# Performance work log

Measured on AMD Instinct MI355X. Metric: run time of the kernel, lower is better.

Reference implementation:

```python
import jax, jax.numpy as jnp
import numpy as np
import itertools

LUT_DIM = 33  # 33x33x33 color LUT, as in Generator3DLUT_zero(dim=33)


def setup_inputs() -> dict:
    key = jax.random.key(0)
    k1, k2 = jax.random.split(key)
    # RGB image batch in [0,1]: [B, 3, H, W]
    x = jax.random.uniform(k1, (4, 3, 1080, 1920), dtype=jnp.float32)
    # Learned LUT parameter: [3, dim, dim, dim] (channels, b-axis, g-axis, r-axis)
    LUT = jax.random.normal(k2, (3, LUT_DIM, LUT_DIM, LUT_DIM), dtype=jnp.float32)
    return {"x": x, "LUT": LUT}


def _trilinear_lut(x, LUT, dim):
    # x: [B,3,H,W] in [0,1]; LUT: [3,dim,dim,dim] indexed [channel, b, g, r]
    # (r varies fastest, matching the original CUDA trilinear_forward kernel
    #  where flat index = r + g*dim + b*dim*dim).
    scaled = jnp.clip(x, 0.0, 1.0) * (dim - 1)          # [B,3,H,W]
    idx = jnp.clip(jnp.floor(scaled).astype(jnp.int32), 0, dim - 2)
    frac = scaled - idx.astype(scaled.dtype)            # in [0,1]
    r_id, g_id, b_id = idx[:, 0], idx[:, 1], idx[:, 2]   # each [B,H,W]
    fr, fg, fb = frac[:, 0], frac[:, 1], frac[:, 2]      # each [B,H,W]

    out = jnp.zeros_like(x)  # [B,3,H,W]
    for dr, dg, db in itertools.product((0, 1), repeat=3):  # 8 corners
        w = (jnp.where(dr, fr, 1.0 - fr)
             * jnp.where(dg, fg, 1.0 - fg)
             * jnp.where(db, fb, 1.0 - fb))               # [B,H,W]
        corner = LUT[:, b_id + db, g_id + dg, r_id + dr]  # [3,B,H,W] gather
        out = out + w[:, None] * jnp.transpose(corner, (1, 0, 2, 3))
    return out


def reference(x, LUT):
    return _trilinear_lut(x, LUT, LUT_DIM)
```

## Files before the change

kernel.cpp:

```cpp
#include <hip/hip_runtime.h>

#define DIM  33
#define DIM2 1089
#define DIM3 35937
#define HW   2073600
#define HW4  518400
#define NPIX 8294400
#define GROUPS (NPIX / 4)
#define CHUNK  4096
#define NCHUNK ((GROUPS + CHUNK - 1) / CHUNK)
#define LDS_BYTES (DIM3 * 4)
#define MAIN_BLOCKS  256
#define MAIN_THREADS 1024

typedef float vf4 __attribute__((ext_vector_type(4)));

#define TBL_OFF 64

__device__ __forceinline__ float ub(unsigned v, int b) {
    return (float)((v >> (8 * b)) & 0xffu);
}

__global__ __launch_bounds__(256) void lut_maxabs_kernel(
        const float* __restrict__ lut, unsigned* __restrict__ maxbits) {
    int i = blockIdx.x * 256 + threadIdx.x;
    float m = 0.0f;
    if (i < 3 * DIM3) m = fabsf(lut[i]);
#pragma unroll
    for (int off = 32; off > 0; off >>= 1)
        m = fmaxf(m, __shfl_down(m, off, 64));
    if ((threadIdx.x & 63) == 0)
        atomicMax(maxbits, __float_as_uint(m));
}

__global__ __launch_bounds__(256) void pack_lut_u8_kernel(
        const float* __restrict__ lut, const unsigned* __restrict__ maxbits,
        unsigned* __restrict__ tbl) {
    int i = blockIdx.x * 256 + threadIdx.x;
    if (i >= DIM3) return;
    float mx  = fmaxf(__uint_as_float(*maxbits), 1e-20f);
    float inv = 127.0f / mx;
    int q0 = min(max(__float2int_rn(lut[i]            * inv) + 128, 0), 255);
    int q1 = min(max(__float2int_rn(lut[i + DIM3]     * inv) + 128, 0), 255);
    int q2 = min(max(__float2int_rn(lut[i + 2 * DIM3] * inv) + 128, 0), 255);
    tbl[i] = (unsigned)q0 | ((unsigned)q1 << 8) | ((unsigned)q2 << 16);
}

extern __shared__ unsigned s_tbl[];

__global__ __launch_bounds__(MAIN_THREADS, 1) void lut_apply_lds(
        const float* __restrict__ x, const unsigned* __restrict__ tbl,
        unsigned* __restrict__ ctr, const unsigned* __restrict__ maxbits,
        float* __restrict__ out) {
    __shared__ unsigned chunk_s;
    for (int i = threadIdx.x; i < DIM3; i += MAIN_THREADS)
        s_tbl[i] = tbl[i];
    __syncthreads();

    const float mx   = fmaxf(__uint_as_float(*maxbits), 1e-20f);
    const float s_   = mx * (1.0f / 127.0f);
    const float bias = -128.0f * s_;

    for (;;) {
        if (threadIdx.x == 0) chunk_s = atomicAdd(ctr, 1u);
        __syncthreads();
        unsigned c = chunk_s;
        __syncthreads();
        if (c >= NCHUNK) return;

        int gend = min((int)((c + 1) * CHUNK), GROUPS);
        for (int g = (int)(c * CHUNK) + threadIdx.x; g < gend; g += MAIN_THREADS) {
            int n   = g / HW4;
            int rem = g - n * HW4;
            size_t base = (size_t)n * (size_t)(3 * HW) + (size_t)rem * 4;

            const vf4 rv = __builtin_nontemporal_load((const vf4*)(x + base));
            const vf4 gv = __builtin_nontemporal_load((const vf4*)(x + base + HW));
            const vf4 bv = __builtin_nontemporal_load((const vf4*)(x + base + 2 * (size_t)HW));

            float oa[4], ob[4], oc[4];
#pragma unroll
            for (int k = 0; k < 4; ++k) {
                float rs = fminf(fmaxf(rv[k], 0.0f), 1.0f) * 32.0f;
                float gs = fminf(fmaxf(gv[k], 0.0f), 1.0f) * 32.0f;
                float bs = fminf(fmaxf(bv[k], 0.0f), 1.0f) * 32.0f;
                int ri = min((int)rs, 31);
                int gi = min((int)gs, 31);
                int bi = min((int)bs, 31);
                float fr = rs - (float)ri;
                float fg = gs - (float)gi;
                float fb = bs - (float)bi;

                int i00 = bi * DIM2 + gi * DIM + ri;
                unsigned c000 = s_tbl[i00];
                unsigned c001 = s_tbl[i00 + 1];
                unsigned c010 = s_tbl[i00 + DIM];
                unsigned c011 = s_tbl[i00 + DIM + 1];
                unsigned c100 = s_tbl[i00 + DIM2];
                unsigned c101 = s_tbl[i00 + DIM2 + 1];
                unsigned c110 = s_tbl[i00 + DIM2 + DIM];
                unsigned c111 = s_tbl[i00 + DIM2 + DIM + 1];

                float wr1 = fr, wr0 = 1.0f - fr;
                float wg1 = fg, wg0 = 1.0f - fg;
                float wb1 = fb, wb0 = 1.0f - fb;
                float wb0g0 = wb0 * wg0, wb0g1 = wb0 * wg1;
                float wb1g0 = wb1 * wg0, wb1g1 = wb1 * wg1;
                float w000 = wb0g0 * wr0, w001 = wb0g0 * wr1;
                float w010 = wb0g1 * wr0, w011 = wb0g1 * wr1;
                float w100 = wb1g0 * wr0, w101 = wb1g0 * wr1;
                float w110 = wb1g1 * wr0, w111 = wb1g1 * wr1;

                float a0, a1, a2;
                a0 =      w000 * ub(c000, 0);
                a1 =      w000 * ub(c000, 1);
                a2 =      w000 * ub(c000, 2);
                a0 = fmaf(w001,  ub(c001, 0), a0);
                a1 = fmaf(w001,  ub(c001, 1), a1);
                a2 = fmaf(w001,  ub(c001, 2), a2);
                a0 = fmaf(w010,  ub(c010, 0), a0);
                a1 = fmaf(w010,  ub(c010, 1), a1);
                a2 = fmaf(w010,  ub(c010, 2), a2);
                a0 = fmaf(w011,  ub(c011, 0), a0);
                a1 = fmaf(w011,  ub(c011, 1), a1);
                a2 = fmaf(w011,  ub(c011, 2), a2);
                a0 = fmaf(w100,  ub(c100, 0), a0);
                a1 = fmaf(w100,  ub(c100, 1), a1);
                a2 = fmaf(w100,  ub(c100, 2), a2);
                a0 = fmaf(w101,  ub(c101, 0), a0);
                a1 = fmaf(w101,  ub(c101, 1), a1);
                a2 = fmaf(w101,  ub(c101, 2), a2);
                a0 = fmaf(w110,  ub(c110, 0), a0);
                a1 = fmaf(w110,  ub(c110, 1), a1);
                a2 = fmaf(w110,  ub(c110, 2), a2);
                a0 = fmaf(w111,  ub(c111, 0), a0);
                a1 = fmaf(w111,  ub(c111, 1), a1);
                a2 = fmaf(w111,  ub(c111, 2), a2);

                oa[k] = fmaf(s_, a0, bias);
                ob[k] = fmaf(s_, a1, bias);
                oc[k] = fmaf(s_, a2, bias);
            }
            vf4 s0 = {oa[0], oa[1], oa[2], oa[3]};
            vf4 s1 = {ob[0], ob[1], ob[2], ob[3]};
            vf4 s2 = {oc[0], oc[1], oc[2], oc[3]};
            __builtin_nontemporal_store(s0, (vf4*)(out + base));
            __builtin_nontemporal_store(s1, (vf4*)(out + base + HW));
            __builtin_nontemporal_store(s2, (vf4*)(out + base + 2 * (size_t)HW));
        }
    }
}

union F4H { vf4 f4; _Float16 h[8]; };

__global__ __launch_bounds__(256) void pack_lut8_kernel(
        const float* __restrict__ lut, vf4* __restrict__ lut8) {
    int i = blockIdx.x * blockDim.x + threadIdx.x;
    if (i >= DIM3) return;
    int b   = i / DIM2;
    int rem = i - b * DIM2;
    int g   = rem / DIM;
    int r   = rem - g * DIM;
    int b1 = min(b + 1, DIM - 1);
    int g1 = min(g + 1, DIM - 1);
    int r1 = min(r + 1, DIM - 1);
    _Float16 h[32];
#pragma unroll
    for (int db = 0; db < 2; ++db)
#pragma unroll
        for (int dg = 0; dg < 2; ++dg)
#pragma unroll
            for (int dr = 0; dr < 2; ++dr) {
                int bb = db ? b1 : b;
                int gg = dg ? g1 : g;
                int rr = dr ? r1 : r;
                int base = bb * DIM2 + gg * DIM + rr;
                int ci = ((db * 2 + dg) * 2 + dr) * 3;
                h[ci + 0] = (_Float16)lut[base];
                h[ci + 1] = (_Float16)lut[base + DIM3];
                h[ci + 2] = (_Float16)lut[base + 2 * DIM3];
            }
#pragma unroll
    for (int k = 24; k < 32; ++k) h[k] = (_Float16)0.0f;
    const vf4* hv = (const vf4*)h;
    vf4* dst = lut8 + (size_t)i * 4;
    dst[0] = hv[0]; dst[1] = hv[1]; dst[2] = hv[2]; dst[3] = hv[3];
}

__global__ __launch_bounds__(256) void lut_apply_fp16x8(
        const float* __restrict__ x, const vf4* __restrict__ lut8,
        float* __restrict__ out) {
    int i4 = blockIdx.x * blockDim.x + threadIdx.x;
    if (i4 >= NPIX / 4) return;
    int n   = i4 / HW4;
    int rem = i4 - n * HW4;
    size_t base = (size_t)n * (size_t)(3 * HW) + (size_t)rem * 4;
    const vf4 rv = __builtin_nontemporal_load((const vf4*)(x + base));
    const vf4 gv = __builtin_nontemporal_load((const vf4*)(x + base + HW));
    const vf4 bv = __builtin_nontemporal_load((const vf4*)(x + base + 2 * (size_t)HW));
    float oa[4], ob[4], oc[4];
#pragma unroll
    for (int k = 0; k < 4; ++k) {
        float rs = fminf(fmaxf(rv[k], 0.0f), 1.0f) * 32.0f;
        float gs = fminf(fmaxf(gv[k], 0.0f), 1.0f) * 32.0f;
        float bs = fminf(fmaxf(bv[k], 0.0f), 1.0f) * 32.0f;
        int ri = min((int)rs, 31);
        int gi = min((int)gs, 31);
        int bi = min((int)bs, 31);
        float fr = rs - (float)ri;
        float fg = gs - (float)gi;
        float fb = bs - (float)bi;
        const vf4* e = lut8 + (size_t)(bi * DIM2 + gi * DIM + ri) * 4;
        F4H q0, q1, q2;
        q0.f4 = e[0]; q1.f4 = e[1]; q2.f4 = e[2];
        float c[24];
#pragma unroll
        for (int j = 0; j < 8; ++j) {
            c[j] = (float)q0.h[j]; c[8 + j] = (float)q1.h[j]; c[16 + j] = (float)q2.h[j];
        }
        float wr[2] = {1.0f - fr, fr};
        float wg[2] = {1.0f - fg, fg};
        float wb[2] = {1.0f - fb, fb};
        float a0 = 0.0f, a1 = 0.0f, a2 = 0.0f;
#pragma unroll
        for (int db = 0; db < 2; ++db)
#pragma unroll
            for (int dg = 0; dg < 2; ++dg) {
                float wbg = wb[db] * wg[dg];
#pragma unroll
                for (int dr = 0; dr < 2; ++dr) {
                    float w = wbg * wr[dr];
                    int ci = ((db * 2 + dg) * 2 + dr) * 3;
                    a0 = fmaf(w, c[ci + 0], a0);
                    a1 = fmaf(w, c[ci + 1], a1);
                    a2 = fmaf(w, c[ci + 2], a2);
                }
            }
        oa[k] = a0; ob[k] = a1; oc[k] = a2;
    }
    vf4 s0 = {oa[0], oa[1], oa[2], oa[3]};
    vf4 s1 = {ob[0], ob[1], ob[2], ob[3]};
    vf4 s2 = {oc[0], oc[1], oc[2], oc[3]};
    __builtin_nontemporal_store(s0, (vf4*)(out + base));
    __builtin_nontemporal_store(s1, (vf4*)(out + base + HW));
    __builtin_nontemporal_store(s2, (vf4*)(out + base + 2 * (size_t)HW));
}

extern "C" void kernel_launch(void* const* d_in, const int* in_sizes, int n_in,
                              void* d_out, int out_size, void* d_ws, size_t ws_size,
                              hipStream_t stream) {
    const float* x   = (const float*)d_in[0];
    const float* lut = (const float*)d_in[1];
    float* out = (float*)d_out;

    unsigned* ctr     = (unsigned*)d_ws;
    unsigned* maxbits = (unsigned*)d_ws + 1;
    unsigned* tbl     = (unsigned*)((char*)d_ws + TBL_OFF);

    static hipError_t attr_err = hipFuncSetAttribute(
        (const void*)lut_apply_lds,
        hipFuncAttributeMaxDynamicSharedMemorySize, LDS_BYTES);
    hipError_t err2 = hipFuncSetAttribute(
        (const void*)lut_apply_lds,
        hipFuncAttributeMaxDynamicSharedMemorySize, LDS_BYTES);

    if (attr_err == hipSuccess && err2 == hipSuccess) {
        hipMemsetAsync(d_ws, 0, 8, stream);
        lut_maxabs_kernel<<<(3 * DIM3 + 255) / 256, 256, 0, stream>>>(lut, maxbits);
        pack_lut_u8_kernel<<<(DIM3 + 255) / 256, 256, 0, stream>>>(lut, maxbits, tbl);
        lut_apply_lds<<<MAIN_BLOCKS, MAIN_THREADS, LDS_BYTES, stream>>>(
            x, tbl, ctr, maxbits, out);
    } else {
        vf4* lut8 = (vf4*)((char*)d_ws + TBL_OFF);
        pack_lut8_kernel<<<(DIM3 + 255) / 256, 256, 0, stream>>>(lut, lut8);
        lut_apply_fp16x8<<<(GROUPS + 255) / 256, 256, 0, stream>>>(x, lut8, out);
    }
}
```

Measured before the change: 202.6 us.

## Fold LUT quantization into main kernel and drop memset and dynamic chunk scheduler

Replaces the memset, the atomic max-abs kernel and the separate pack kernel with a per-block max kernel that writes partial maxima to slots. The main kernel now reduces those maxima itself and quantizes the LUT straight into LDS. The atomic chunk counter is also replaced by a static grid-stride loop. This removes two launches plus the per-chunk barriers and atomics. In exchange every block repeats the LUT quantization from global memory, and static scheduling can leave some blocks finishing later than others.

Measured after the change: 188.1 us. -7.2%, faster.

```diff
diff --git a/kernel.cpp b/kernel.cpp
--- a/kernel.cpp
+++ b/kernel.cpp
@@ -7,11 +7,10 @@
 #define HW4  518400
 #define NPIX 8294400
 #define GROUPS (NPIX / 4)
-#define CHUNK  4096
-#define NCHUNK ((GROUPS + CHUNK - 1) / CHUNK)
 #define LDS_BYTES (DIM3 * 4)
 #define MAIN_BLOCKS  256
 #define MAIN_THREADS 1024
+#define NB_MAX ((3 * DIM3 + 255) / 256)
 
 typedef float vf4 __attribute__((ext_vector_type(4)));
 
@@ -21,133 +20,131 @@
     return (float)((v >> (8 * b)) & 0xffu);
 }
 
-__global__ __launch_bounds__(256) void lut_maxabs_kernel(
-        const float* __restrict__ lut, unsigned* __restrict__ maxbits) {
+__global__ __launch_bounds__(256) void lut_maxabs_blocks(
+        const float* __restrict__ lut, float* __restrict__ slots) {
+    __shared__ float red[4];
     int i = blockIdx.x * 256 + threadIdx.x;
     float m = 0.0f;
     if (i < 3 * DIM3) m = fabsf(lut[i]);
 #pragma unroll
     for (int off = 32; off > 0; off >>= 1)
         m = fmaxf(m, __shfl_down(m, off, 64));
-    if ((threadIdx.x & 63) == 0)
-        atomicMax(maxbits, __float_as_uint(m));
-}
-
-__global__ __launch_bounds__(256) void pack_lut_u8_kernel(
-        const float* __restrict__ lut, const unsigned* __restrict__ maxbits,
-        unsigned* __restrict__ tbl) {
-    int i = blockIdx.x * 256 + threadIdx.x;
-    if (i >= DIM3) return;
-    float mx  = fmaxf(__uint_as_float(*maxbits), 1e-20f);
-    float inv = 127.0f / mx;
-    int q0 = min(max(__float2int_rn(lut[i]            * inv) + 128, 0), 255);
-    int q1 = min(max(__float2int_rn(lut[i + DIM3]     * inv) + 128, 0), 255);
-    int q2 = min(max(__float2int_rn(lut[i + 2 * DIM3] * inv) + 128, 0), 255);
-    tbl[i] = (unsigned)q0 | ((unsigned)q1 << 8) | ((unsigned)q2 << 16);
+    if ((threadIdx.x & 63) == 0) red[threadIdx.x >> 6] = m;
+    __syncthreads();
+    if (threadIdx.x == 0)
+        slots[blockIdx.x] = fmaxf(fmaxf(red[0], red[1]), fmaxf(red[2], red[3]));
 }
 
 extern __shared__ unsigned s_tbl[];
 
 __global__ __launch_bounds__(MAIN_THREADS, 1) void lut_apply_lds(
-        const float* __restrict__ x, const unsigned* __restrict__ tbl,
-        unsigned* __restrict__ ctr, const unsigned* __restrict__ maxbits,
-        float* __restrict__ out) {
-    __shared__ unsigned chunk_s;
-    for (int i = threadIdx.x; i < DIM3; i += MAIN_THREADS)
-        s_tbl[i] = tbl[i];
+        const float* __restrict__ x, const float* __restrict__ lut,
+        const float* __restrict__ slots, float* __restrict__ out) {
+    __shared__ float red[16];
+
+    float m = 0.0f;
+    if (threadIdx.x < NB_MAX) m = slots[threadIdx.x];
+#pragma unroll
+    for (int off = 32; off > 0; off >>= 1)
+        m = fmaxf(m, __shfl_down(m, off, 64));
+    if ((threadIdx.x & 63) == 0) red[threadIdx.x >> 6] = m;
     __syncthreads();
-
-    const float mx   = fmaxf(__uint_as_float(*maxbits), 1e-20f);
+    float mx = red[0];
+#pragma unroll
+    for (int j = 1; j < 16; ++j) mx = fmaxf(mx, red[j]);
+    mx = fmaxf(mx, 1e-20f);
+
+    const float inv = 127.0f / mx;
+    for (int i = threadIdx.x; i < DIM3; i += MAIN_THREADS) {
+        int q0 = min(max(__float2int_rn(lut[i]            * inv) + 128, 0), 255);
+        int q1 = min(max(__float2int_rn(lut[i + DIM3]     * inv) + 128, 0), 255);
+        int q2 = min(max(__float2int_rn(lut[i + 2 * DIM3] * inv) + 128, 0), 255);
+        s_tbl[i] = (unsigned)q0 | ((unsigned)q1 << 8) | ((unsigned)q2 << 16);
+    }
+    __syncthreads();
+
     const float s_   = mx * (1.0f / 127.0f);
     const float bias = -128.0f * s_;
 
-    for (;;) {
-        if (threadIdx.x == 0) chunk_s = atomicAdd(ctr, 1u);
-        __syncthreads();
-        unsigned c = chunk_s;
-        __syncthreads();
-        if (c >= NCHUNK) return;
-
-        int gend = min((int)((c + 1) * CHUNK), GROUPS);
-        for (int g = (int)(c * CHUNK) + threadIdx.x; g < gend; g += MAIN_THREADS) {
-            int n   = g / HW4;
-            int rem = g - n * HW4;
-            size_t base = (size_t)n * (size_t)(3 * HW) + (size_t)rem * 4;
-
-            const vf4 rv = __builtin_nontemporal_load((const vf4*)(x + base));
-            const vf4 gv = __builtin_nontemporal_load((const vf4*)(x + base + HW));
-            const vf4 bv = __builtin_nontemporal_load((const vf4*)(x + base + 2 * (size_t)HW));
-
-            float oa[4], ob[4], oc[4];
-#pragma unroll
-            for (int k = 0; k < 4; ++k) {
-                float rs = fminf(fmaxf(rv[k], 0.0f), 1.0f) * 32.0f;
-                float gs = fminf(fmaxf(gv[k], 0.0f), 1.0f) * 32.0f;
-                float bs = fminf(fmaxf(bv[k], 0.0f), 1.0f) * 32.0f;
-                int ri = min((int)rs, 31);
-                int gi = min((int)gs, 31);
-                int bi = min((int)bs, 31);
-                float fr = rs - (float)ri;
-                float fg = gs - (float)gi;
-                float fb = bs - (float)bi;
-
-                int i00 = bi * DIM2 + gi * DIM + ri;
-                unsigned c000 = s_tbl[i00];
-                unsigned c001 = s_tbl[i00 + 1];
-                unsigned c010 = s_tbl[i00 + DIM];
-                unsigned c011 = s_tbl[i00 + DIM + 1];
-                unsigned c100 = s_tbl[i00 + DIM2];
-                unsigned c101 = s_tbl[i00 + DIM2 + 1];
-                unsigned c110 = s_tbl[i00 + DIM2 + DIM];
-                unsigned c111 = s_tbl[i00 + DIM2 + DIM + 1];
-
-                float wr1 = fr, wr0 = 1.0f - fr;
-                float wg1 = fg, wg0 = 1.0f - fg;
-                float wb1 = fb, wb0 = 1.0f - fb;
-                float wb0g0 = wb0 * wg0, wb0g1 = wb0 * wg1;
-                float wb1g0 = wb1 * wg0, wb1g1 = wb1 * wg1;
-                float w000 = wb0g0 * wr0, w001 = wb0g0 * wr1;
-                float w010 = wb0g1 * wr0, w011 = wb0g1 * wr1;
-                float w100 = wb1g0 * wr0, w101 = wb1g0 * wr1;
-                float w110 = wb1g1 * wr0, w111 = wb1g1 * wr1;
-
-                float a0, a1, a2;
-                a0 =      w000 * ub(c000, 0);
-                a1 =      w000 * ub(c000, 1);
-                a2 =      w000 * ub(c000, 2);
-                a0 = fmaf(w001,  ub(c001, 0), a0);
-                a1 = fmaf(w001,  ub(c001, 1), a1);
-                a2 = fmaf(w001,  ub(c001, 2), a2);
-                a0 = fmaf(w010,  ub(c010, 0), a0);
-                a1 = fmaf(w010,  ub(c010, 1), a1);
-                a2 = fmaf(w010,  ub(c010, 2), a2);
-                a0 = fmaf(w011,  ub(c011, 0), a0);
-                a1 = fmaf(w011,  ub(c011, 1), a1);
-                a2 = fmaf(w011,  ub(c011, 2), a2);
-                a0 = fmaf(w100,  ub(c100, 0), a0);
-                a1 = fmaf(w100,  ub(c100, 1), a1);
-                a2 = fmaf(w100,  ub(c100, 2), a2);
-                a0 = fmaf(w101,  ub(c101, 0), a0);
-                a1 = fmaf(w101,  ub(c101, 1), a1);
-                a2 = fmaf(w101,  ub(c101, 2), a2);
-                a0 = fmaf(w110,  ub(c110, 0), a0);
-                a1 = fmaf(w110,  ub(c110, 1), a1);
-                a2 = fmaf(w110,  ub(c110, 2), a2);
-                a0 = fmaf(w111,  ub(c111, 0), a0);
-                a1 = fmaf(w111,  ub(c111, 1), a1);
-                a2 = fmaf(w111,  ub(c111, 2), a2);
-
-                oa[k] = fmaf(s_, a0, bias);
-                ob[k] = fmaf(s_, a1, bias);
-                oc[k] = fmaf(s_, a2, bias);
-            }
-            vf4 s0 = {oa[0], oa[1], oa[2], oa[3]};
-            vf4 s1 = {ob[0], ob[1], ob[2], ob[3]};
-            vf4 s2 = {oc[0], oc[1], oc[2], oc[3]};
-            __builtin_nontemporal_store(s0, (vf4*)(out + base));
-            __builtin_nontemporal_store(s1, (vf4*)(out + base + HW));
-            __builtin_nontemporal_store(s2, (vf4*)(out + base + 2 * (size_t)HW));
+    for (int g = blockIdx.x * MAIN_THREADS + threadIdx.x; g < GROUPS;
+         g += MAIN_BLOCKS * MAIN_THREADS) {
+        int n   = g / HW4;
+        int rem = g - n * HW4;
+        size_t base = (size_t)n * (size_t)(3 * HW) + (size_t)rem * 4;
+
+        const vf4 rv = __builtin_nontemporal_load((const vf4*)(x + base));
+        const vf4 gv = __builtin_nontemporal_load((const vf4*)(x + base + HW));
+        const vf4 bv = __builtin_nontemporal_load((const vf4*)(x + base + 2 * (size_t)HW));
+
+        float oa[4], ob[4], oc[4];
+#pragma unroll
+        for (int k = 0; k < 4; ++k) {
+            float rs = fminf(fmaxf(rv[k], 0.0f), 1.0f) * 32.0f;
+            float gs = fminf(fmaxf(gv[k], 0.0f), 1.0f) * 32.0f;
+            float bs = fminf(fmaxf(bv[k], 0.0f), 1.0f) * 32.0f;
+            int ri = min((int)rs, 31);
+            int gi = min((int)gs, 31);
+            int bi = min((int)bs, 31);
+            float fr = rs - (float)ri;
+            float fg = gs - (float)gi;
+            float fb = bs - (float)bi;
+
+            int i00 = bi * DIM2 + gi * DIM + ri;
+            unsigned c000 = s_tbl[i00];
+            unsigned c001 = s_tbl[i00 + 1];
+            unsigned c010 = s_tbl[i00 + DIM];
+            unsigned c011 = s_tbl[i00 + DIM + 1];
+            unsigned c100 = s_tbl[i00 + DIM2];
+            unsigned c101 = s_tbl[i00 + DIM2 + 1];
+            unsigned c110 = s_tbl[i00 + DIM2 + DIM];
+            unsigned c111 = s_tbl[i00 + DIM2 + DIM + 1];
+
+            float wr1 = fr, wr0 = 1.0f - fr;
+            float wg1 = fg, wg0 = 1.0f - fg;
+            float wb1 = fb, wb0 = 1.0f - fb;
+            float wb0g0 = wb0 * wg0, wb0g1 = wb0 * wg1;
+            float wb1g0 = wb1 * wg0, wb1g1 = wb1 * wg1;
+            float w000 = wb0g0 * wr0, w001 = wb0g0 * wr1;
+            float w010 = wb0g1 * wr0, w011 = wb0g1 * wr1;
+            float w100 = wb1g0 * wr0, w101 = wb1g0 * wr1;
+            float w110 = wb1g1 * wr0, w111 = wb1g1 * wr1;
+
+            float a0, a1, a2;
+            a0 =      w000 * ub(c000, 0);
+            a1 =      w000 * ub(c000, 1);
+            a2 =      w000 * ub(c000, 2);
+            a0 = fmaf(w001,  ub(c001, 0), a0);
+            a1 = fmaf(w001,  ub(c001, 1), a1);
+            a2 = fmaf(w001,  ub(c001, 2), a2);
+            a0 = fmaf(w010,  ub(c010, 0), a0);
+            a1 = fmaf(w010,  ub(c010, 1), a1);
+            a2 = fmaf(w010,  ub(c010, 2), a2);
+            a0 = fmaf(w011,  ub(c011, 0), a0);
+            a1 = fmaf(w011,  ub(c011, 1), a1);
+            a2 = fmaf(w011,  ub(c011, 2), a2);
+            a0 = fmaf(w100,  ub(c100, 0), a0);
+            a1 = fmaf(w100,  ub(c100, 1), a1);
+            a2 = fmaf(w100,  ub(c100, 2), a2);
+            a0 = fmaf(w101,  ub(c101, 0), a0);
+            a1 = fmaf(w101,  ub(c101, 1), a1);
+            a2 = fmaf(w101,  ub(c101, 2), a2);
+            a0 = fmaf(w110,  ub(c110, 0), a0);
+            a1 = fmaf(w110,  ub(c110, 1), a1);
+            a2 = fmaf(w110,  ub(c110, 2), a2);
+            a0 = fmaf(w111,  ub(c111, 0), a0);
+            a1 = fmaf(w111,  ub(c111, 1), a1);
+            a2 = fmaf(w111,  ub(c111, 2), a2);
+
+            oa[k] = fmaf(s_, a0, bias);
+            ob[k] = fmaf(s_, a1, bias);
+            oc[k] = fmaf(s_, a2, bias);
         }
+        vf4 s0 = {oa[0], oa[1], oa[2], oa[3]};
+        vf4 s1 = {ob[0], ob[1], ob[2], ob[3]};
+        vf4 s2 = {oc[0], oc[1], oc[2], oc[3]};
+        __builtin_nontemporal_store(s0, (vf4*)(out + base));
+        __builtin_nontemporal_store(s1, (vf4*)(out + base + HW));
+        __builtin_nontemporal_store(s2, (vf4*)(out + base + 2 * (size_t)HW));
     }
 }
 
@@ -253,9 +250,7 @@
     const float* lut = (const float*)d_in[1];
     float* out = (float*)d_out;
 
-    unsigned* ctr     = (unsigned*)d_ws;
-    unsigned* maxbits = (unsigned*)d_ws + 1;
-    unsigned* tbl     = (unsigned*)((char*)d_ws + TBL_OFF);
+    float* slots = (float*)((char*)d_ws + TBL_OFF);
 
     static hipError_t attr_err = hipFuncSetAttribute(
         (const void*)lut_apply_lds,
@@ -265,11 +260,9 @@
         hipFuncAttributeMaxDynamicSharedMemorySize, LDS_BYTES);
 
     if (attr_err == hipSuccess && err2 == hipSuccess) {
-        hipMemsetAsync(d_ws, 0, 8, stream);
-        lut_maxabs_kernel<<<(3 * DIM3 + 255) / 256, 256, 0, stream>>>(lut, maxbits);
-        pack_lut_u8_kernel<<<(DIM3 + 255) / 256, 256, 0, stream>>>(lut, maxbits, tbl);
+        lut_maxabs_blocks<<<NB_MAX, 256, 0, stream>>>(lut, slots);
         lut_apply_lds<<<MAIN_BLOCKS, MAIN_THREADS, LDS_BYTES, stream>>>(
-            x, tbl, ctr, maxbits, out);
+            x, lut, slots, out);
     } else {
         vf4* lut8 = (vf4*)((char*)d_ws + TBL_OFF);
         pack_lut8_kernel<<<(DIM3 + 255) / 256, 256, 0, stream>>>(lut, lut8);
```
